# Kernel optimization log

Hardware: AMD Instinct MI355X
Metric: run time of the kernel (lower is better)

The kernel has to match this reference:

```python
import jax, jax.numpy as jnp
import numpy as np

EMB = 1024

def setup_inputs() -> dict:
    key = jax.random.key(0)
    ks = jax.random.split(key, 6)
    T, k1, k2, D = 64, 256, 1024, EMB
    scale = 1.0 / np.sqrt(D)
    return {
        "fast_feature": jax.random.normal(ks[0], (T, k2, D), jnp.float32),
        "slow_feature": jax.random.normal(ks[1], (T, k1, D), jnp.float32),
        "fast_W": jax.random.normal(ks[2], (D, D), jnp.float32) * scale,
        "fast_b": jax.random.normal(ks[3], (D,), jnp.float32) * 0.01,
        "slow_W": jax.random.normal(ks[4], (D, D), jnp.float32) * scale,
        "slow_b": jax.random.normal(ks[5], (D,), jnp.float32) * 0.01,
    }

def reference(fast_feature, slow_feature, fast_W, fast_b, slow_W, slow_b):
    # Linear projections (torch Linear: x @ W.T + b)
    fast_key = jnp.einsum('tkd,ed->tke', fast_feature, fast_W) + fast_b  # [T,k2,D]
    slow_key = jnp.einsum('tkd,ed->tke', slow_feature, slow_W) + slow_b  # [T,k1,D]
    # Scaled dot-product similarity fast->slow
    sim = jnp.einsum('tqd,tkd->tqk', fast_key, slow_key)  # [T,k2,k1]
    sim = sim / jnp.sqrt(jnp.asarray(slow_feature.shape[-1], sim.dtype))
    attn = jax.nn.softmax(sim, axis=-1)
    ctx = jnp.einsum('tqk,tkd->tqd', attn, slow_feature)  # note: values are raw slow_feature
    return fast_feature + ctx
```

## Files before the change

### kernel.cpp

```cpp
#include <hip/hip_runtime.h>
#include <stdint.h>

typedef __attribute__((ext_vector_type(8))) short bf16x8;
typedef __attribute__((ext_vector_type(4))) float f32x4;

__device__ __forceinline__ unsigned short f2bf(float f) {
  unsigned int u = __builtin_bit_cast(unsigned int, f);
  u += 0x7FFFu + ((u >> 16) & 1u);
  return (unsigned short)(u >> 16);
}

__device__ __forceinline__ float bf2f(unsigned short s) {
  return __builtin_bit_cast(float, (unsigned int)s << 16);
}

__device__ __forceinline__ void gload_lds16(const void* g, void* l) {
  __builtin_amdgcn_global_load_lds(
      (__attribute__((address_space(1))) void*)(uintptr_t)g,
      (__attribute__((address_space(3))) void*)l,
      16, 0, 0);
}

#define BARRIER() do { asm volatile("" ::: "memory"); __builtin_amdgcn_s_barrier(); asm volatile("" ::: "memory"); } while (0)
#define WAITVM(N) asm volatile("s_waitcnt vmcnt(" #N ")" ::: "memory")

template <int MODE>
__global__ __launch_bounds__(512, 2) void gemm8(
    const unsigned short* __restrict__ A, const unsigned short* __restrict__ B,
    void* __restrict__ Cv, const void* __restrict__ aux, int N, int K,
    int nm, int nn, long sAB, long sBB, long sCB, long sXB, float scale)
{
  __shared__ __align__(16) char lds[131072];
  char* ldsc = lds;

  const int tid = threadIdx.x;
  const int lane = tid & 63;
  const int wid = tid >> 6;
  const int fr = lane & 15, fq = lane >> 4;

  const int nwg = gridDim.x;
  const int id = blockIdx.x;
  const int swz = (id & 7) * (nwg >> 3) + (id >> 3);
  const int per = nm * nn;
  const int t = swz / per;
  const int rem = swz - t * per;
  const int mi_ = rem / nn, ni_ = rem - mi_ * nn;
  const long bm = (long)mi_ * 256, bn = (long)ni_ * 256;

  const unsigned short* Ag = A + (long)t * sAB + bm * K;
  const unsigned short* Bg = B + (long)t * sBB + bn * K;
  const int NT = K >> 6;

  const unsigned short* aS[2][2];
  const unsigned short* bS[2][2];
#pragma unroll
  for (int p = 0; p < 2; ++p) {
    const int q = p * 512 + tid;
    const int lr = q >> 3, cs = q & 7;
    const int cl = cs ^ (lr & 7);
#pragma unroll
    for (int h = 0; h < 2; ++h) {
      const int gA = ((lr >> 6) << 7) | (h << 6) | (lr & 63);
      const int gB = ((lr >> 5) << 6) | (h << 5) | (lr & 31);
      aS[p][h] = Ag + (long)gA * K + cl * 8;
      bS[p][h] = Bg + (long)gB * K + cl * 8;
    }
  }

  const int c0 = ((fq ^ (fr & 3)) + ((fr >> 2) & 1) * 4) * 16;
  const int aRd = ((wid >> 2) * 64 + fr) * 128 + c0;
  const int bRd = ((wid & 3) * 32 + fr) * 128 + c0;

  f32x4 acc[2][2][4][2];
#pragma unroll
  for (int a = 0; a < 2; a++)
#pragma unroll
    for (int b = 0; b < 2; b++)
#pragma unroll
      for (int i = 0; i < 4; i++)
#pragma unroll
        for (int j = 0; j < 2; j++)
#pragma unroll
          for (int r = 0; r < 4; r++) acc[a][b][i][j][r] = 0.f;

  bf16x8 af0[4][2], af1[4][2], bf[2][2][2];

#define STAGE(srcArr, aoff, h, ktv, b) do {                                   \
  _Pragma("unroll")                                                           \
  for (int p = 0; p < 2; ++p)                                                 \
    gload_lds16(srcArr[p][h] + ((long)(ktv) << 6),                            \
                ldsc + (aoff) + ((b) << 16) + ((h) << 14) + (p << 13) + (wid << 10)); \
} while (0)

#define LDA(dst, mi, cub) do {                                                \
  _Pragma("unroll")                                                           \
  for (int i = 0; i < 4; ++i) {                                               \
    dst[i][0] = *(const bf16x8*)(ldsc + (cub) + (mi) * 16384 + aRd + i * 2048);        \
    dst[i][1] = *(const bf16x8*)(ldsc + (cub) + (mi) * 16384 + (aRd ^ 64) + i * 2048); \
  }                                                                           \
} while (0)

#define LDB(nj, cub) do {                                                     \
  _Pragma("unroll")                                                           \
  for (int j = 0; j < 2; ++j) {                                               \
    bf[nj][j][0] = *(const bf16x8*)(ldsc + 32768 + (cub) + (nj) * 16384 + bRd + j * 2048);        \
    bf[nj][j][1] = *(const bf16x8*)(ldsc + 32768 + (cub) + (nj) * 16384 + (bRd ^ 64) + j * 2048); \
  }                                                                           \
} while (0)

#define QUAD(AF, mi, nj) do {                                                 \
  __builtin_amdgcn_s_setprio(1);                                              \
  _Pragma("unroll")                                                           \
  for (int i = 0; i < 4; ++i)                                                 \
  _Pragma("unroll")                                                           \
  for (int j = 0; j < 2; ++j) {                                               \
    acc[mi][nj][i][j] = __builtin_amdgcn_mfma_f32_16x16x32_bf16(              \
        AF[i][0], bf[nj][j][0], acc[mi][nj][i][j], 0, 0, 0);                  \
    acc[mi][nj][i][j] = __builtin_amdgcn_mfma_f32_16x16x32_bf16(              \
        AF[i][1], bf[nj][j][1], acc[mi][nj][i][j], 0, 0, 0);                  \
  }                                                                           \
  __builtin_amdgcn_s_setprio(0);                                              \
} while (0)

  STAGE(aS, 0, 0, 0, 0);
  STAGE(bS, 32768, 0, 0, 0);
  STAGE(bS, 32768, 1, 0, 0);
  STAGE(aS, 0, 1, 0, 0);
  if (NT > 1) {
    STAGE(aS, 0, 0, 1, 1);
    STAGE(bS, 32768, 0, 1, 1);
    STAGE(bS, 32768, 1, 1, 1);
    WAITVM(6);
  } else {
    WAITVM(0);
  }
  BARRIER();

  for (int kt = 0; kt < NT; ++kt) {
    const int cur = kt & 1, nxt = cur ^ 1;
    const int cub = cur << 16;
    LDA(af0, 0, cub);
    LDB(0, cub);
    if (kt + 1 < NT) STAGE(aS, 0, 1, kt + 1, nxt);
    BARRIER();
    QUAD(af0, 0, 0);
    BARRIER();
    LDB(1, cub);
    LDA(af1, 1, cub);
    if (kt + 2 < NT) {
      STAGE(aS, 0, 0, kt + 2, cur);
      STAGE(bS, 32768, 0, kt + 2, cur);
    }
    BARRIER();
    QUAD(af0, 0, 1);
    QUAD(af1, 1, 0);
    BARRIER();
    if (kt + 2 < NT) {
      STAGE(bS, 32768, 1, kt + 2, cur);
      QUAD(af1, 1, 1);
      WAITVM(6);
    } else {
      QUAD(af1, 1, 1);
      WAITVM(0);
    }
    BARRIER();
  }

  if (MODE == 1) {
    float* red  = (float*)ldsc;
    float* red2 = (float*)(ldsc + 4096);
    const int wc = wid & 3;
    const int rbase = (wid >> 2) * 128;
#pragma unroll
    for (int mi = 0; mi < 2; ++mi)
#pragma unroll
      for (int i = 0; i < 4; ++i)
#pragma unroll
        for (int r = 0; r < 4; ++r) {
          float m = fmaxf(fmaxf(acc[mi][0][i][0][r], acc[mi][0][i][1][r]),
                          fmaxf(acc[mi][1][i][0][r], acc[mi][1][i][1][r]));
#pragma unroll
          for (int o = 1; o <= 8; o <<= 1) m = fmaxf(m, __shfl_xor(m, o));
          if (fr == 0) red[(rbase + mi * 64 + i * 16 + fq * 4 + r) * 4 + wc] = m;
        }
    BARRIER();
#pragma unroll
    for (int mi = 0; mi < 2; ++mi)
#pragma unroll
      for (int i = 0; i < 4; ++i)
#pragma unroll
        for (int r = 0; r < 4; ++r) {
          const int rl = rbase + mi * 64 + i * 16 + fq * 4 + r;
          f32x4 mm = *(f32x4*)&red[rl * 4];
          const float M = fmaxf(fmaxf(mm[0], mm[1]), fmaxf(mm[2], mm[3]));
          float s = 0.f;
#pragma unroll
          for (int nj = 0; nj < 2; ++nj)
#pragma unroll
            for (int j = 0; j < 2; ++j) {
              float e = __expf((acc[mi][nj][i][j][r] - M) * scale);
              acc[mi][nj][i][j][r] = e;
              s += e;
            }
#pragma unroll
          for (int o = 1; o <= 8; o <<= 1) s += __shfl_xor(s, o);
          if (fr == 0) red2[rl * 4 + wc] = s;
        }
    BARRIER();
    unsigned short* C = (unsigned short*)Cv + (long)t * sCB;
#pragma unroll
    for (int mi = 0; mi < 2; ++mi)
#pragma unroll
      for (int i = 0; i < 4; ++i)
#pragma unroll
        for (int r = 0; r < 4; ++r) {
          const int rl = rbase + mi * 64 + i * 16 + fq * 4 + r;
          f32x4 sv = *(f32x4*)&red2[rl * 4];
          const float inv = 1.0f / (sv[0] + sv[1] + sv[2] + sv[3]);
          const long gr = bm + rl;
#pragma unroll
          for (int nj = 0; nj < 2; ++nj)
#pragma unroll
            for (int j = 0; j < 2; ++j) {
              const long gcol = bn + wc * 64 + nj * 32 + j * 16 + fr;
              C[gr * N + gcol] = f2bf(acc[mi][nj][i][j][r] * inv);
            }
        }
  } else {
#pragma unroll
    for (int mi = 0; mi < 2; ++mi)
#pragma unroll
      for (int nj = 0; nj < 2; ++nj)
#pragma unroll
        for (int i = 0; i < 4; ++i) {
          const long grow0 = bm + (wid >> 2) * 128 + mi * 64 + i * 16 + fq * 4;
#pragma unroll
          for (int j = 0; j < 2; ++j) {
            const long gcol = bn + (wid & 3) * 64 + nj * 32 + j * 16 + fr;
            if (MODE == 0) {
              unsigned short* C = (unsigned short*)Cv + (long)t * sCB;
              const float bv = ((const float*)aux)[gcol];
#pragma unroll
              for (int r = 0; r < 4; ++r)
                C[(grow0 + r) * N + gcol] = f2bf(acc[mi][nj][i][j][r] + bv);
            } else {
              float* C = (float*)Cv + (long)t * sCB;
              const unsigned short* X = (const unsigned short*)aux + (long)t * sXB;
#pragma unroll
              for (int r = 0; r < 4; ++r) {
                const long idx = (grow0 + r) * N + gcol;
                C[idx] = acc[mi][nj][i][j][r] + bf2f(X[idx]);
              }
            }
          }
        }
  }
#undef STAGE
#undef LDA
#undef LDB
#undef QUAD
}

__global__ __launch_bounds__(256) void convert_f32_bf16(
    const float* __restrict__ in, unsigned short* __restrict__ out, long n) {
  long i = ((long)blockIdx.x * 256 + threadIdx.x) * 4;
  long stride = (long)gridDim.x * 1024;
  for (; i < n; i += stride) {
    float4 v = *(const float4*)(in + i);
    ushort4 o;
    o.x = f2bf(v.x); o.y = f2bf(v.y); o.z = f2bf(v.z); o.w = f2bf(v.w);
    *(ushort4*)(out + i) = o;
  }
}

__global__ __launch_bounds__(256) void convert_weights(
    const float* __restrict__ in1, unsigned short* __restrict__ out1,
    const float* __restrict__ in2, unsigned short* __restrict__ out2) {
  const int half = blockIdx.x >> 9;
  const float* in = half ? in2 : in1;
  unsigned short* out = half ? out2 : out1;
  long i = ((long)(blockIdx.x & 511) * 256 + threadIdx.x) * 4;
  long stride = 512L * 1024;
  for (; i < 1048576L; i += stride) {
    float4 v = *(const float4*)(in + i);
    ushort4 o;
    o.x = f2bf(v.x); o.y = f2bf(v.y); o.z = f2bf(v.z); o.w = f2bf(v.w);
    *(ushort4*)(out + i) = o;
  }
}

__global__ __launch_bounds__(256) void convert_transpose_slow(
    const float* __restrict__ in, unsigned short* __restrict__ outR,
    unsigned short* __restrict__ outT) {
  __shared__ unsigned short tile[32][33];
  int t = blockIdx.z;
  int d0 = blockIdx.x * 32;
  int k0 = blockIdx.y * 32;
  const float* ip = in + (long)t * 256 * 1024;
  unsigned short* rp = outR + (long)t * 256 * 1024;
  unsigned short* tp = outT + (long)t * 1024 * 256;
  int tx = threadIdx.x & 31, ty = threadIdx.x >> 5;
#pragma unroll
  for (int p = 0; p < 4; p++) {
    int k = ty + p * 8;
    unsigned short b = f2bf(ip[(long)(k0 + k) * 1024 + d0 + tx]);
    tile[k][tx] = b;
    rp[(long)(k0 + k) * 1024 + d0 + tx] = b;
  }
  __syncthreads();
#pragma unroll
  for (int p = 0; p < 4; p++) {
    int d = ty + p * 8;
    tp[(long)(d0 + d) * 256 + k0 + tx] = tile[tx][d];
  }
}

extern "C" void kernel_launch(void* const* d_in, const int* in_sizes, int n_in,
                              void* d_out, int out_size, void* d_ws, size_t ws_size,
                              hipStream_t stream) {
  const float* fastF     = (const float*)d_in[0];
  const float* slowF     = (const float*)d_in[1];
  const float* fastW     = (const float*)d_in[2];
  const float* fast_bias = (const float*)d_in[3];
  const float* slowW     = (const float*)d_in[4];
  const float* slow_bias = (const float*)d_in[5];
  float* out = (float*)d_out;

  char* ws = (char*)d_ws;
  unsigned short* fastBf  = (unsigned short*)(ws);
  unsigned short* fastKey = (unsigned short*)(ws + 134217728L);
  unsigned short* slowBf  = (unsigned short*)(ws + 268435456L);
  unsigned short* attnBf  = (unsigned short*)(ws + 268435456L);
  unsigned short* slowT   = (unsigned short*)(ws + 301989888L);
  unsigned short* slowKey = (unsigned short*)(ws + 335544320L);
  unsigned short* fWb     = (unsigned short*)(ws + 369098752L);
  unsigned short* sWb     = (unsigned short*)(ws + 371195904L);

  convert_f32_bf16<<<2048, 256, 0, stream>>>(fastF, fastBf, 67108864L);
  convert_weights<<<1024, 256, 0, stream>>>(fastW, fWb, slowW, sWb);
  convert_transpose_slow<<<dim3(32, 8, 64), 256, 0, stream>>>(slowF, slowBf, slowT);

  gemm8<0><<<64 * 4, 512, 0, stream>>>(slowBf, sWb, slowKey, slow_bias,
      1024, 1024, 64, 4, 0, 0, 0, 0, 1.f);
  gemm8<0><<<256 * 4, 512, 0, stream>>>(fastBf, fWb, fastKey, fast_bias,
      1024, 1024, 256, 4, 0, 0, 0, 0, 1.f);
  gemm8<1><<<4 * 1 * 64, 512, 0, stream>>>(fastKey, slowKey, attnBf, nullptr,
      256, 1024, 4, 1, 1048576L, 262144L, 262144L, 0, 0.03125f);
  gemm8<2><<<4 * 4 * 64, 512, 0, stream>>>(attnBf, slowT, out, fastBf,
      1024, 256, 4, 4, 262144L, 262144L, 1048576L, 1048576L, 1.f);
}
```

Baseline: 472.7 us.

## Replace generic context GEMM with dedicated small-tile K=256 kernel

```diff
diff --git a/kernel.cpp b/kernel.cpp
--- a/kernel.cpp
+++ b/kernel.cpp
@@ -237,21 +237,11 @@
 #pragma unroll
           for (int j = 0; j < 2; ++j) {
             const long gcol = bn + (wid & 3) * 64 + nj * 32 + j * 16 + fr;
-            if (MODE == 0) {
-              unsigned short* C = (unsigned short*)Cv + (long)t * sCB;
-              const float bv = ((const float*)aux)[gcol];
-#pragma unroll
-              for (int r = 0; r < 4; ++r)
-                C[(grow0 + r) * N + gcol] = f2bf(acc[mi][nj][i][j][r] + bv);
-            } else {
-              float* C = (float*)Cv + (long)t * sCB;
-              const unsigned short* X = (const unsigned short*)aux + (long)t * sXB;
-#pragma unroll
-              for (int r = 0; r < 4; ++r) {
-                const long idx = (grow0 + r) * N + gcol;
-                C[idx] = acc[mi][nj][i][j][r] + bf2f(X[idx]);
-              }
-            }
+            unsigned short* C = (unsigned short*)Cv + (long)t * sCB;
+            const float bv = ((const float*)aux)[gcol];
+#pragma unroll
+            for (int r = 0; r < 4; ++r)
+              C[(grow0 + r) * N + gcol] = f2bf(acc[mi][nj][i][j][r] + bv);
           }
         }
   }
@@ -259,6 +249,107 @@
 #undef LDA
 #undef LDB
 #undef QUAD
+}
+
+__global__ __launch_bounds__(512, 2) void ctx_v2(
+    const unsigned short* __restrict__ attn,
+    const unsigned short* __restrict__ slowT,
+    float* __restrict__ out,
+    const unsigned short* __restrict__ resid)
+{
+  __shared__ __align__(16) char lds[65536];
+  char* ldsc = lds;
+
+  const int tid = threadIdx.x;
+  const int lane = tid & 63;
+  const int wid = tid >> 6;
+  const int fr = lane & 15, fq = lane >> 4;
+
+  const int nwg = gridDim.x;
+  const int id = blockIdx.x;
+  const int swz = (id & 7) * (nwg >> 3) + (id >> 3);
+  const int t = swz >> 6;
+  const int rem = swz & 63;
+  const int mi_ = rem >> 3, ni_ = rem & 7;
+  const long bm = (long)mi_ * 128, bn = (long)ni_ * 128;
+
+  const unsigned short* Ag = attn + (long)t * 262144 + bm * 256;
+  const unsigned short* Bg = slowT + (long)t * 262144;
+
+  {
+    const int gRow = wid * 8 + (lane >> 3);
+    const int cs = lane & 7;
+#pragma unroll
+    for (int p = 0; p < 2; ++p) {
+      const int r = p * 64 + gRow;
+      const int cl = cs ^ (r & 7);
+      const unsigned short* src = Ag + (long)r * 256 + cl * 8;
+#pragma unroll
+      for (int s = 0; s < 4; ++s)
+        gload_lds16(src + s * 64,
+                    ldsc + s * 16384 + p * 8192 + wid * 1024 + (lane & 63) * 16);
+    }
+  }
+
+  bf16x8 bB[2][8];
+  {
+    const long col0 = bn + (wid & 3) * 32 + fr;
+#pragma unroll
+    for (int nj = 0; nj < 2; ++nj) {
+      const unsigned short* bp = Bg + (col0 + nj * 16) * 256 + fq * 8;
+#pragma unroll
+      for (int kk = 0; kk < 8; ++kk)
+        bB[nj][kk] = *(const bf16x8*)(bp + kk * 32);
+    }
+  }
+
+  WAITVM(0);
+  BARRIER();
+
+  f32x4 acc[4][2];
+#pragma unroll
+  for (int i = 0; i < 4; i++)
+#pragma unroll
+    for (int j = 0; j < 2; j++)
+#pragma unroll
+      for (int r = 0; r < 4; r++) acc[i][j][r] = 0.f;
+
+  const int c0 = ((fq ^ (fr & 3)) + ((fr >> 2) & 1) * 4) * 16;
+  const int rowb = ((wid >> 2) * 64 + fr) * 128 + c0;
+
+#pragma unroll
+  for (int kk = 0; kk < 8; ++kk) {
+    const int sub = (kk >> 1) * 16384;
+    const int flip = (kk & 1) ? 64 : 0;
+    bf16x8 aF[4];
+#pragma unroll
+    for (int mif = 0; mif < 4; ++mif)
+      aF[mif] = *(const bf16x8*)(ldsc + sub + ((rowb + mif * 2048) ^ flip));
+    __builtin_amdgcn_s_setprio(1);
+#pragma unroll
+    for (int mif = 0; mif < 4; ++mif)
+#pragma unroll
+      for (int nj = 0; nj < 2; ++nj)
+        acc[mif][nj] = __builtin_amdgcn_mfma_f32_16x16x32_bf16(
+            aF[mif], bB[nj][kk], acc[mif][nj], 0, 0, 0);
+    __builtin_amdgcn_s_setprio(0);
+  }
+
+  float* C = out + (long)t * 1048576;
+  const unsigned short* X = resid + (long)t * 1048576;
+#pragma unroll
+  for (int mif = 0; mif < 4; ++mif) {
+    const long grow0 = bm + (wid >> 2) * 64 + mif * 16 + fq * 4;
+#pragma unroll
+    for (int nj = 0; nj < 2; ++nj) {
+      const long gcol = bn + (wid & 3) * 32 + nj * 16 + fr;
+#pragma unroll
+      for (int r = 0; r < 4; ++r) {
+        const long idx = (grow0 + r) * 1024 + gcol;
+        C[idx] = acc[mif][nj][r] + bf2f(X[idx]);
+      }
+    }
+  }
 }
 
 __global__ __launch_bounds__(256) void convert_f32_bf16(
@@ -346,6 +437,5 @@
       1024, 1024, 256, 4, 0, 0, 0, 0, 1.f);
   gemm8<1><<<4 * 1 * 64, 512, 0, stream>>>(fastKey, slowKey, attnBf, nullptr,
       256, 1024, 4, 1, 1048576L, 262144L, 262144L, 0, 0.03125f);
-  gemm8<2><<<4 * 4 * 64, 512, 0, stream>>>(attnBf, slowT, out, fastBf,
-      1024, 256, 4, 4, 262144L, 262144L, 1048576L, 1048576L, 1.f);
-}
+  ctx_v2<<<4096, 512, 0, stream>>>(attnBf, slowT, out, fastBf);
+}
```

Result: slower. 496.4 us (+5.0%).
